# Performance work log

Hardware: AMD Instinct MI355X
Metric: run time of the kernel (lower is better)

The kernel has to match this reference:

```python
import jax, jax.numpy as jnp
import numpy as np

B, T, D = 2, 2048, 2048
H, HD, RD = 16, 192, 64
CD = HD - RD          # 128 content dims per head
QR, DL = 768, 512     # q lora rank, kv latent dim
THETA = 10000.0


def setup_inputs() -> dict:
    key = jax.random.key(0)
    ks = jax.random.split(key, 9)
    s = 0.02
    return {
        "x": jax.random.normal(ks[0], (B, T, D), jnp.float32),
        "wq_down": jax.random.normal(ks[1], (D, QR), jnp.float32) * s,
        "wq_up": jax.random.normal(ks[2], (QR, H * CD), jnp.float32) * s,
        "wq_rope": jax.random.normal(ks[3], (D, H * RD), jnp.float32) * s,
        "wkv_down": jax.random.normal(ks[4], (D, DL), jnp.float32) * s,
        "wk_up": jax.random.normal(ks[5], (DL, H * CD), jnp.float32) * s,
        "wv_up": jax.random.normal(ks[6], (DL, H * HD), jnp.float32) * s,
        "wk_rope": jax.random.normal(ks[7], (D, H * RD), jnp.float32) * s,
        "wo": jax.random.normal(ks[8], (H * HD, D), jnp.float32) * s,
    }


def _rope_tables(seq_len):
    inv = 1.0 / (THETA ** (jnp.arange(0, RD, 2, dtype=jnp.float32) / RD))  # [RD/2]
    ang = jnp.arange(seq_len, dtype=jnp.float32)[:, None] * inv[None, :]  # [T, RD/2]
    return jnp.cos(ang), jnp.sin(ang)


def _apply_rope(x, cos, sin):
    # x: [B,H,T,RD]; cos/sin: [T,RD/2] broadcast over B,H
    d = RD // 2
    x1, x2 = x[..., :d], x[..., d:]
    return jnp.concatenate([x1 * cos - x2 * sin, x1 * sin + x2 * cos], axis=-1)


def reference(x, wq_down, wq_up, wq_rope, wkv_down, wk_up, wv_up, wk_rope, wo):
    # projections
    q_c = (x @ wq_down) @ wq_up                       # [B,T,H*CD]
    q_p = x @ wq_rope                                 # [B,T,H*RD]
    latent = x @ wkv_down                             # [B,T,DL]
    k_c = latent @ wk_up                              # [B,T,H*CD]
    k_p = x @ wk_rope                                 # [B,T,H*RD]
    v = latent @ wv_up                                # [B,T,H*HD]

    def heads(t, d):
        return t.reshape(B, T, H, d).transpose(0, 2, 1, 3)  # [B,H,T,d]

    q_c, q_p = heads(q_c, CD), heads(q_p, RD)
    k_c, k_p = heads(k_c, CD), heads(k_p, RD)
    v = heads(v, HD)

    cos, sin = _rope_tables(T)
    q_p = _apply_rope(q_p, cos, sin)
    k_p = _apply_rope(k_p, cos, sin)

    q = jnp.concatenate([q_c, q_p], axis=-1)          # [B,H,T,HD]
    k = jnp.concatenate([k_c, k_p], axis=-1)          # [B,H,T,HD]

    scale = 1.0 / jnp.sqrt(jnp.asarray(HD, q.dtype))
    scores = jnp.einsum("bhqd,bhkd->bhqk", q, k) * scale
    causal = jnp.tril(jnp.ones((T, T), dtype=bool))
    scores = jnp.where(causal, scores, jnp.finfo(scores.dtype).min)
    attn = jax.nn.softmax(scores, axis=-1)
    out = jnp.einsum("bhqk,bhkd->bhqd", attn, v)      # [B,H,T,HD]
    out = out.transpose(0, 2, 1, 3).reshape(B, T, H * HD)
    return out @ wo                                   # [B,T,D]
```

## Files before the change

### kernel.cpp

```cpp
#include <hip/hip_runtime.h>
#include <hip/hip_bf16.h>
#include <cstdint>
#include <cstddef>

typedef __bf16 bf16_t;
typedef __bf16 bf16x8 __attribute__((ext_vector_type(8)));
typedef float f32x4 __attribute__((ext_vector_type(4)));

#define MFMA16(a, b, c) __builtin_amdgcn_mfma_f32_16x16x32_bf16((a), (b), (c), 0, 0, 0)

__device__ __forceinline__ void gload_lds16(const void* g, void* l) {
  __builtin_amdgcn_global_load_lds((__attribute__((address_space(1))) void*)(g),
                                   (__attribute__((address_space(3))) void*)(l),
                                   16, 0, 0);
}

__device__ __forceinline__ uint32_t pkbf(float lo, float hi) {
  union { bf16_t h[2]; uint32_t u; } u2;
  u2.h[0] = (bf16_t)lo; u2.h[1] = (bf16_t)hi;
  return u2.u;
}

__global__ __launch_bounds__(256) void cvt_f32_to_bf16(const float* __restrict__ in,
                                                       bf16_t* __restrict__ out) {
  size_t i = ((size_t)blockIdx.x * 256 + threadIdx.x) * 4;
  float4 v = *(const float4*)(in + i);
  bf16_t o[4] = {(bf16_t)v.x, (bf16_t)v.y, (bf16_t)v.z, (bf16_t)v.w};
  *(uint2*)(out + i) = *(uint2*)o;
}

__global__ __launch_bounds__(256) void transpose_all(
    const float* __restrict__ s0, const float* __restrict__ s1,
    const float* __restrict__ s2, const float* __restrict__ s3,
    const float* __restrict__ s4, const float* __restrict__ s5,
    const float* __restrict__ s6, const float* __restrict__ s7,
    bf16_t* __restrict__ t0, bf16_t* __restrict__ t1, bf16_t* __restrict__ t2,
    bf16_t* __restrict__ t3, bf16_t* __restrict__ t4, bf16_t* __restrict__ t5,
    bf16_t* __restrict__ t6, bf16_t* __restrict__ t7) {
  __shared__ bf16_t tile[32][33];
  const int lid = blockIdx.x;
  const float* src; bf16_t* dst; int R, C, bx, by;
  if (lid < 1536)       { src=s0; dst=t0; R=2048; C=768;  int lo=lid;        bx=lo%24; by=lo/24; }
  else if (lid < 2560)  { src=s1; dst=t1; R=2048; C=512;  int lo=lid-1536;   bx=lo%16; by=lo/16; }
  else if (lid < 4608)  { src=s2; dst=t2; R=2048; C=1024; int lo=lid-2560;   bx=lo%32; by=lo/32; }
  else if (lid < 6656)  { src=s3; dst=t3; R=2048; C=1024; int lo=lid-4608;   bx=lo%32; by=lo/32; }
  else if (lid < 8192)  { src=s4; dst=t4; R=768;  C=2048; int lo=lid-6656;   bx=lo%64; by=lo/64; }
  else if (lid < 9216)  { src=s5; dst=t5; R=512;  C=2048; int lo=lid-8192;   bx=lo%64; by=lo/64; }
  else if (lid < 10752) { src=s6; dst=t6; R=512;  C=3072; int lo=lid-9216;   bx=lo%96; by=lo/96; }
  else                  { src=s7; dst=t7; R=3072; C=2048; int lo=lid-10752;  bx=lo%64; by=lo/64; }
  const int c0 = bx * 32, r0 = by * 32;
  const int tx = threadIdx.x, ty = threadIdx.y;
#pragma unroll
  for (int s = 0; s < 4; s++) {
    int r = ty + s * 8;
    tile[r][tx] = (bf16_t)src[(size_t)(r0 + r) * C + c0 + tx];
  }
  __syncthreads();
#pragma unroll
  for (int s = 0; s < 4; s++) {
    int r = ty + s * 8;
    dst[(size_t)(c0 + r) * R + r0 + tx] = tile[tx][r];
  }
}

__global__ __launch_bounds__(256) void rope_both(bf16_t* __restrict__ qb,
                                                 bf16_t* __restrict__ kb) {
  const int gid = blockIdx.x;
  bf16_t* buf = (gid < 8192) ? qb : kb;
  int idx = (gid & 8191) * 256 + threadIdx.x;
  int j = idx & 31;
  int h = (idx >> 5) & 15;
  int row = idx >> 9;
  int t = row & 2047;
  size_t base = (size_t)row * 3072 + h * 192 + 128;
  float inv = expf(-(float)j * 0.28782313662425574f);
  float ang = (float)t * inv;
  float c, s;
  sincosf(ang, &s, &c);
  float x1 = (float)buf[base + j];
  float x2 = (float)buf[base + j + 32];
  buf[base + j]      = (bf16_t)(x1 * c - x2 * s);
  buf[base + j + 32] = (bf16_t)(x1 * s + x2 * c);
}

template <int MODE>
__global__ __launch_bounds__(512, 2) void gemm_bt2(const bf16_t* __restrict__ A, int lda,
                                                   const bf16_t* __restrict__ Bt,
                                                   void* __restrict__ C0, void* __restrict__ C1,
                                                   void* __restrict__ C2, int K, int ldc) {
  __shared__ __align__(16) bf16_t sA0[256 * 64];
  __shared__ __align__(16) bf16_t sB0[128 * 64];
  __shared__ __align__(16) bf16_t sA1[256 * 64];
  __shared__ __align__(16) bf16_t sB1[128 * 64];
  const int tid = threadIdx.x;
  const int l = tid & 63, w = tid >> 6;
  const int l15 = l & 15, l4 = (l >> 4) & 3;
  const int wr = w >> 1, wc = w & 1;
  const int m0 = blockIdx.y * 256, n0 = blockIdx.x * 128;
  const int nt = K >> 6;

  f32x4 acc[4][4] = {};

#define STAGEG(SA, SB, KT)                                                          \
  {                                                                                 \
    const int kts = (KT) * 64;                                                      \
    _Pragma("unroll")                                                               \
    for (int r = 0; r < 4; r++) {                                                   \
      int i = r * 512 + tid;                                                        \
      int row = i >> 3, cl = i & 7;                                                 \
      int cg = cl ^ (row & 7);                                                      \
      gload_lds16(A + (size_t)(m0 + row) * lda + kts + cg * 8,                      \
                  (char*)(SA) + (size_t)(r * 512 + w * 64) * 16);                   \
    }                                                                               \
    _Pragma("unroll")                                                               \
    for (int r = 0; r < 2; r++) {                                                   \
      int i = r * 512 + tid;                                                        \
      int row = i >> 3, cl = i & 7;                                                 \
      int cg = cl ^ (row & 7);                                                      \
      gload_lds16(Bt + (size_t)(n0 + row) * K + kts + cg * 8,                       \
                  (char*)(SB) + (size_t)(r * 512 + w * 64) * 16);                   \
    }                                                                               \
  }

#define GCOMPUTE(SA, SB)                                                            \
  {                                                                                 \
    _Pragma("unroll")                                                               \
    for (int ks = 0; ks < 2; ks++) {                                                \
      bf16x8 af[4], bfr[4];                                                         \
      _Pragma("unroll")                                                             \
      for (int mf = 0; mf < 4; mf++) {                                              \
        int row = wr * 64 + mf * 16 + l15;                                          \
        int cl = (ks * 4 + l4) ^ (row & 7);                                         \
        af[mf] = *(const bf16x8*)((SA) + row * 64 + cl * 8);                        \
      }                                                                             \
      _Pragma("unroll")                                                             \
      for (int nf = 0; nf < 4; nf++) {                                              \
        int row = wc * 64 + nf * 16 + l15;                                          \
        int cl = (ks * 4 + l4) ^ (row & 7);                                         \
        bfr[nf] = *(const bf16x8*)((SB) + row * 64 + cl * 8);                       \
      }                                                                             \
      _Pragma("unroll")                                                             \
      for (int mf = 0; mf < 4; mf++)                                                \
        _Pragma("unroll")                                                           \
        for (int nf = 0; nf < 4; nf++)                                              \
          acc[mf][nf] = MFMA16(af[mf], bfr[nf], acc[mf][nf]);                       \
    }                                                                               \
  }

  STAGEG(sA0, sB0, 0)
  for (int t = 0; t < nt; t += 2) {
    STAGEG(sA1, sB1, t + 1)
    asm volatile("s_waitcnt vmcnt(6)\n\ts_barrier" ::: "memory");
    GCOMPUTE(sA0, sB0)
    asm volatile("s_barrier" ::: "memory");
    if (t + 2 < nt) {
      STAGEG(sA0, sB0, t + 2)
      asm volatile("s_waitcnt vmcnt(6)\n\ts_barrier" ::: "memory");
    } else {
      asm volatile("s_waitcnt vmcnt(0)\n\ts_barrier" ::: "memory");
    }
    GCOMPUTE(sA1, sB1)
    asm volatile("s_barrier" ::: "memory");
  }
#undef STAGEG
#undef GCOMPUTE

#pragma unroll
  for (int mf = 0; mf < 4; mf++)
#pragma unroll
    for (int nf = 0; nf < 4; nf++) {
      const int mbase = m0 + wr * 64 + mf * 16 + l4 * 4;
      const int n = n0 + wc * 64 + nf * 16 + l15;
      if constexpr (MODE == 1) {
#pragma unroll
        for (int r = 0; r < 4; r++)
          ((float*)C0)[(size_t)(mbase + r) * ldc + n] = acc[mf][nf][r];
      } else if constexpr (MODE == 2) {
#pragma unroll
        for (int r = 0; r < 4; r++)
          ((bf16_t*)C0)[(size_t)(mbase + r) * 3072 + (n >> 7) * 192 + (n & 127)] =
              (bf16_t)acc[mf][nf][r];
      } else if constexpr (MODE == 4) {
        if (n < 1280) {
#pragma unroll
          for (int r = 0; r < 4; r++)
            ((bf16_t*)C0)[(size_t)(mbase + r) * 1280 + n] = (bf16_t)acc[mf][nf][r];
        } else if (n < 2304) {
          int nn = n - 1280;
#pragma unroll
          for (int r = 0; r < 4; r++)
            ((bf16_t*)C1)[(size_t)(mbase + r) * 3072 + (nn >> 6) * 192 + 128 + (nn & 63)] =
                (bf16_t)acc[mf][nf][r];
        } else {
          int nn = n - 2304;
#pragma unroll
          for (int r = 0; r < 4; r++)
            ((bf16_t*)C2)[(size_t)(mbase + r) * 3072 + (nn >> 6) * 192 + 128 + (nn & 63)] =
                (bf16_t)acc[mf][nf][r];
        }
      } else {
        if (n < 2048) {
#pragma unroll
          for (int r = 0; r < 4; r++)
            ((bf16_t*)C0)[(size_t)(mbase + r) * 3072 + (n >> 7) * 192 + (n & 127)] =
                (bf16_t)acc[mf][nf][r];
        } else {
          int nn = n - 2048;
          int hh = nn / 192, dd = nn - hh * 192;
          int bb = mbase >> 11, tt = mbase & 2047;
          bf16_t pk4[4] = {(bf16_t)acc[mf][nf][0], (bf16_t)acc[mf][nf][1],
                           (bf16_t)acc[mf][nf][2], (bf16_t)acc[mf][nf][3]};
          *(uint2*)((bf16_t*)C1 + ((size_t)(bb * 16 + hh) * 192 + dd) * 2048 + tt) =
              *(uint2*)pk4;
        }
      }
    }
}

__global__ __launch_bounds__(512, 2) void attn_kernel(const bf16_t* __restrict__ q,
                                                      const bf16_t* __restrict__ kbuf,
                                                      const bf16_t* __restrict__ vt,
                                                      bf16_t* __restrict__ ao) {
  __shared__ __align__(16) bf16_t sK0[64][192];
  __shared__ __align__(16) bf16_t sK1[64][192];
  __shared__ __align__(16) bf16_t sV0[192][64];
  __shared__ __align__(16) bf16_t sV1[192][64];

  const int tid = threadIdx.x, l = tid & 63, w = tid >> 6;
  const int l15 = l & 15, l4 = (l >> 4) & 3;
  const int bh = blockIdx.x & 31;
  const int c = blockIdx.x >> 5;
  const int b = bh >> 4, h = bh & 15;
  const int ca = c, cb = 15 - c;
  const int ra = ca * 128 + w * 16;
  const int rb = cb * 128 + w * 16;
  const int tga = 2 * ca + (w >> 2);
  const int tgb = 2 * cb + (w >> 2);

  const bf16_t* qp = q + (size_t)b * 2048 * 3072 + h * 192;
  const bf16_t* kp = kbuf + (size_t)b * 2048 * 3072 + h * 192;
  const bf16_t* vp = vt + (size_t)bh * 192 * 2048;

  bf16x8 qf[2][6];
#pragma unroll
  for (int kd = 0; kd < 6; kd++) {
    qf[0][kd] = *(const bf16x8*)(qp + (size_t)(ra + l15) * 3072 + kd * 32 + l4 * 8);
    qf[1][kd] = *(const bf16x8*)(qp + (size_t)(rb + l15) * 3072 + kd * 32 + l4 * 8);
  }

  f32x4 o[2][12] = {};
  float mrow[2] = {-__builtin_inff(), -__builtin_inff()};
  float lrow[2] = {0.0f, 0.0f};

  const float scale = 0.07216878364870322f;
  const float THR = 7.0f;
  const int nkt = 2 * cb + 2;
  const int src0 = l15 + ((l4 & 1) << 5);
  const int src1 = src0 + 16;
  const bool hibank = (l4 & 2) != 0;

#define STAGE(SK, SV, KT)                                                           \
  {                                                                                 \
    const int k0s = (KT) * 64;                                                      \
    _Pragma("unroll")                                                               \
    for (int r = 0; r < 3; r++) {                                                   \
      int i = r * 512 + tid;                                                        \
      int row = i / 24, cc = i % 24;                                                \
      int g = cc - (row & 7) * 3;                                                   \
      if (g < 0) g += 24;                                                           \
      gload_lds16(kp + (size_t)(k0s + row) * 3072 + g * 8,                          \
                  (char*)&SK[0][0] + (size_t)(r * 512 + w * 64) * 16);              \
    }                                                                               \
    _Pragma("unroll")                                                               \
    for (int r = 0; r < 3; r++) {                                                   \
      int i = r * 512 + tid;                                                        \
      int d = i >> 3, cc = i & 7;                                                   \
      gload_lds16(vp + (size_t)d * 2048 + k0s + (cc ^ (d & 7)) * 8,                 \
                  (char*)&SV[0][0] + (size_t)(r * 512 + w * 64) * 16);              \
    }                                                                               \
  }

#define SOFTMAX_CHUNK(c, rbase, tg)                                                    \
    {                                                                                  \
      const bool diag = (kt == (tg));                                                  \
      _Pragma("unroll")                                                                \
      for (int nf = 0; nf < 4; nf++)                                                   \
        _Pragma("unroll")                                                              \
        for (int r = 0; r < 4; r++) {                                                  \
          float sv = s[c][nf][r] * scale;                                              \
          if (diag) {                                                                  \
            int ktok = k0 + nf * 16 + l4 * 4 + r;                                      \
            if (ktok > (rbase) + l15) sv = -__builtin_inff();                          \
          }                                                                            \
          s[c][nf][r] = sv;                                                            \
        }                                                                              \
      float m_in = s[c][0][0];                                                         \
      _Pragma("unroll")                                                                \
      for (int nf = 0; nf < 4; nf++)                                                   \
        _Pragma("unroll")                                                              \
        for (int r = 0; r < 4; r++)                                                    \
          if (nf | r) m_in = fmaxf(m_in, s[c][nf][r]);                                 \
      m_in = fmaxf(m_in, __shfl_xor(m_in, 16));                                        \
      m_in = fmaxf(m_in, __shfl_xor(m_in, 32));                                        \
      if (!__all(m_in - mrow[c] <= THR)) {                                             \
        float mn = fmaxf(mrow[c], m_in);                                               \
        float alpha = __expf(mrow[c] - mn);                                            \
        mrow[c] = mn;                                                                  \
        lrow[c] *= alpha;                                                              \
        f32x4 av;                                                                      \
        _Pragma("unroll")                                                              \
        for (int r = 0; r < 4; r++) av[r] = __shfl(alpha, l4 * 4 + r);                 \
        _Pragma("unroll")                                                              \
        for (int nf2 = 0; nf2 < 12; nf2++) o[c][nf2] *= av;                            \
      }                                                                                \
      float rs = 0.0f;                                                                 \
      _Pragma("unroll")                                                                \
      for (int nf = 0; nf < 4; nf++)                                                   \
        _Pragma("unroll")                                                              \
        for (int r = 0; r < 4; r++) {                                                  \
          float pv = __expf(s[c][nf][r] - mrow[c]);                                    \
          s[c][nf][r] = pv;                                                            \
          rs += pv;                                                                    \
        }                                                                              \
      rs += __shfl_xor(rs, 16);                                                        \
      rs += __shfl_xor(rs, 32);                                                        \
      lrow[c] += rs;                                                                   \
      uint32_t wq[8];                                                                  \
      _Pragma("unroll")                                                                \
      for (int nf = 0; nf < 4; nf++) {                                                 \
        wq[nf * 2 + 0] = pkbf(s[c][nf][0], s[c][nf][1]);                               \
        wq[nf * 2 + 1] = pkbf(s[c][nf][2], s[c][nf][3]);                               \
      }                                                                                \
      _Pragma("unroll")                                                                \
      for (int ks = 0; ks < 2; ks++) {                                                 \
        uint32_t A0 = __shfl(wq[(2 * ks) * 2 + 0], src0);                              \
        uint32_t A1 = __shfl(wq[(2 * ks) * 2 + 1], src0);                              \
        uint32_t B0 = __shfl(wq[(2 * ks + 1) * 2 + 0], src0);                          \
        uint32_t B1 = __shfl(wq[(2 * ks + 1) * 2 + 1], src0);                          \
        uint32_t C0w = __shfl(wq[(2 * ks) * 2 + 0], src1);                             \
        uint32_t C1w = __shfl(wq[(2 * ks) * 2 + 1], src1);                             \
        uint32_t D0 = __shfl(wq[(2 * ks + 1) * 2 + 0], src1);                          \
        uint32_t D1 = __shfl(wq[(2 * ks + 1) * 2 + 1], src1);                          \
        union { uint32_t u[4]; bf16x8 v; } fr;                                         \
        fr.u[0] = hibank ? B0 : A0;                                                    \
        fr.u[1] = hibank ? B1 : A1;                                                    \
        fr.u[2] = hibank ? D0 : C0w;                                                   \
        fr.u[3] = hibank ? D1 : C1w;                                                   \
        pa[c][ks] = fr.v;                                                              \
      }                                                                                \
    }

#define TILE_BODY(SK, SV, KT)                                                          \
  {                                                                                    \
    const int kt = (KT);                                                               \
    const int k0 = kt * 64;                                                            \
    const bool act_a = (kt <= tga);                                                    \
    const bool act_b = (kt <= tgb);                                                    \
    f32x4 s[2][4] = {};                                                                \
    _Pragma("unroll")                                                                  \
    for (int kd = 0; kd < 6; kd++) {                                                   \
      bf16x8 bk[4];                                                                    \
      _Pragma("unroll")                                                                \
      for (int nf = 0; nf < 4; nf++) {                                                 \
        int row = nf * 16 + l15;                                                       \
        int cl = kd * 4 + l4 + (row & 7) * 3;                                          \
        if (cl >= 24) cl -= 24;                                                        \
        bk[nf] = *(const bf16x8*)(&SK[row][cl * 8]);                                   \
      }                                                                                \
      if (act_b) {                                                                     \
        _Pragma("unroll")                                                              \
        for (int nf = 0; nf < 4; nf++)                                                 \
          s[1][nf] = MFMA16(bk[nf], qf[1][kd], s[1][nf]);                              \
      }                                                                                \
      if (act_a) {                                                                     \
        _Pragma("unroll")                                                              \
        for (int nf = 0; nf < 4; nf++)                                                 \
          s[0][nf] = MFMA16(bk[nf], qf[0][kd], s[0][nf]);                              \
      }                                                                                \
    }                                                                                  \
    bf16x8 pa[2][2] = {};                                                              \
    if (act_b) SOFTMAX_CHUNK(1, rb, tgb)                                               \
    if (act_a) SOFTMAX_CHUNK(0, ra, tga)                                               \
    _Pragma("unroll")                                                                  \
    for (int ks = 0; ks < 2; ks++) {                                                   \
      _Pragma("unroll")                                                                \
      for (int nf2 = 0; nf2 < 12; nf2++) {                                             \
        int d = nf2 * 16 + l15;                                                        \
        int cl = (ks * 4 + l4) ^ (d & 7);                                              \
        bf16x8 vb = *(const bf16x8*)(&SV[d][cl * 8]);                                  \
        if (act_b) o[1][nf2] = MFMA16(pa[1][ks], vb, o[1][nf2]);                       \
        if (act_a) o[0][nf2] = MFMA16(pa[0][ks], vb, o[0][nf2]);                       \
      }                                                                                \
    }                                                                                  \
  }

  STAGE(sK0, sV0, 0)
  __syncthreads();

  for (int kt0 = 0; kt0 < nkt; kt0 += 2) {
    STAGE(sK1, sV1, kt0 + 1)
    TILE_BODY(sK0, sV0, kt0)
    __syncthreads();
    if (kt0 + 2 < nkt) STAGE(sK0, sV0, kt0 + 2)
    TILE_BODY(sK1, sV1, kt0 + 1)
    __syncthreads();
  }
#undef STAGE
#undef SOFTMAX_CHUNK
#undef TILE_BODY

#pragma unroll
  for (int mf = 0; mf < 2; mf++) {
    const int rbase = (mf == 0) ? ra : rb;
#pragma unroll
    for (int r = 0; r < 4; r++) {
      float lv = __shfl(lrow[mf], l4 * 4 + r);
      float inv = 1.0f / lv;
      int qrow = rbase + l4 * 4 + r;
#pragma unroll
      for (int nf2 = 0; nf2 < 12; nf2++) {
        int d = nf2 * 16 + l15;
        ao[(size_t)(b * 2048 + qrow) * 3072 + h * 192 + d] = (bf16_t)(o[mf][nf2][r] * inv);
      }
    }
  }
}

extern "C" void kernel_launch(void* const* d_in, const int* in_sizes, int n_in,
                              void* d_out, int out_size, void* d_ws, size_t ws_size,
                              hipStream_t stream) {
  const float* x       = (const float*)d_in[0];
  const float* wq_down = (const float*)d_in[1];
  const float* wq_up   = (const float*)d_in[2];
  const float* wq_rope = (const float*)d_in[3];
  const float* wkv_down= (const float*)d_in[4];
  const float* wk_up   = (const float*)d_in[5];
  const float* wv_up   = (const float*)d_in[6];
  const float* wk_rope = (const float*)d_in[7];
  const float* wo      = (const float*)d_in[8];
  float* out = (float*)d_out;

  char* p = (char*)d_ws;
  auto take = [&](size_t elems) { bf16_t* r = (bf16_t*)p; p += elems * 2; return r; };
  bf16_t* xb    = take(4096ull * 2048);
  bf16_t* fw1   = take(3328ull * 2048);
  bf16_t* wqu_t = take(2048ull * 768);
  bf16_t* fw2   = take(5120ull * 512);
  bf16_t* wo_t  = take(2048ull * 3072);
  bf16_t* qkvd  = take(4096ull * 1280);
  bf16_t* qbuf  = take(4096ull * 3072);
  bf16_t* kbuf  = take(4096ull * 3072);
  bf16_t* ao    = take(4096ull * 3072);
  bf16_t* vt    = take(4096ull * 3072);

  dim3 tb(32, 8);
  cvt_f32_to_bf16<<<8192, 256, 0, stream>>>(x, xb);
  transpose_all<<<16896, tb, 0, stream>>>(
      wq_down, wkv_down, wq_rope, wk_rope, wq_up, wk_up, wv_up, wo,
      fw1, fw1 + 768ull * 2048, fw1 + 1280ull * 2048, fw1 + 2304ull * 2048,
      wqu_t, fw2, fw2 + 2048ull * 512, wo_t);

  gemm_bt2<4><<<dim3(26, 16), 512, 0, stream>>>(xb, 2048, fw1, qkvd, qbuf, kbuf, 2048, 0);
  gemm_bt2<2><<<dim3(16, 16), 512, 0, stream>>>(qkvd, 1280, wqu_t, qbuf, nullptr, nullptr, 768, 0);
  gemm_bt2<5><<<dim3(40, 16), 512, 0, stream>>>(qkvd + 768, 1280, fw2, kbuf, vt, nullptr, 512, 0);

  rope_both<<<16384, 256, 0, stream>>>(qbuf, kbuf);

  attn_kernel<<<256, 512, 0, stream>>>(qbuf, kbuf, vt, ao);

  gemm_bt2<1><<<dim3(16, 16), 512, 0, stream>>>(ao, 3072, wo_t, out, nullptr, nullptr, 3072, 2048);
}
```

Measured before the change: 347.1 us.

## Triple-buffer GEMM LDS with interleaved loads and MFMA priority boosting

The GEMM main loop moves from a double-buffered scheme to a three-stage LDS ring. Each k-tile is split into four sub-phases, and the prefetch of tile t+2 is spread across those phases between barriers. s_setprio raises wave priority around the MFMA bursts in both the GEMM and the attention kernel, to encourage compute/memory overlap across waves. LDS use grows to 144 KB per block, so the launch bound of two blocks per CU may no longer hold, and the extra barriers add synchronization cost.

```diff
diff --git a/kernel.cpp b/kernel.cpp
--- a/kernel.cpp
+++ b/kernel.cpp
@@ -89,9 +89,11 @@
                                                    void* __restrict__ C0, void* __restrict__ C1,
                                                    void* __restrict__ C2, int K, int ldc) {
   __shared__ __align__(16) bf16_t sA0[256 * 64];
+  __shared__ __align__(16) bf16_t sA1[256 * 64];
+  __shared__ __align__(16) bf16_t sA2[256 * 64];
   __shared__ __align__(16) bf16_t sB0[128 * 64];
-  __shared__ __align__(16) bf16_t sA1[256 * 64];
   __shared__ __align__(16) bf16_t sB1[128 * 64];
+  __shared__ __align__(16) bf16_t sB2[128 * 64];
   const int tid = threadIdx.x;
   const int l = tid & 63, w = tid >> 6;
   const int l15 = l & 15, l4 = (l >> 4) & 3;
@@ -101,69 +103,115 @@
 
   f32x4 acc[4][4] = {};
 
-#define STAGEG(SA, SB, KT)                                                          \
-  {                                                                                 \
-    const int kts = (KT) * 64;                                                      \
-    _Pragma("unroll")                                                               \
-    for (int r = 0; r < 4; r++) {                                                   \
-      int i = r * 512 + tid;                                                        \
-      int row = i >> 3, cl = i & 7;                                                 \
-      int cg = cl ^ (row & 7);                                                      \
-      gload_lds16(A + (size_t)(m0 + row) * lda + kts + cg * 8,                      \
-                  (char*)(SA) + (size_t)(r * 512 + w * 64) * 16);                   \
-    }                                                                               \
-    _Pragma("unroll")                                                               \
-    for (int r = 0; r < 2; r++) {                                                   \
-      int i = r * 512 + tid;                                                        \
-      int row = i >> 3, cl = i & 7;                                                 \
-      int cg = cl ^ (row & 7);                                                      \
-      gload_lds16(Bt + (size_t)(n0 + row) * K + kts + cg * 8,                       \
-                  (char*)(SB) + (size_t)(r * 512 + w * 64) * 16);                   \
-    }                                                                               \
-  }
-
-#define GCOMPUTE(SA, SB)                                                            \
-  {                                                                                 \
-    _Pragma("unroll")                                                               \
-    for (int ks = 0; ks < 2; ks++) {                                                \
-      bf16x8 af[4], bfr[4];                                                         \
-      _Pragma("unroll")                                                             \
-      for (int mf = 0; mf < 4; mf++) {                                              \
-        int row = wr * 64 + mf * 16 + l15;                                          \
-        int cl = (ks * 4 + l4) ^ (row & 7);                                         \
-        af[mf] = *(const bf16x8*)((SA) + row * 64 + cl * 8);                        \
-      }                                                                             \
-      _Pragma("unroll")                                                             \
-      for (int nf = 0; nf < 4; nf++) {                                              \
-        int row = wc * 64 + nf * 16 + l15;                                          \
-        int cl = (ks * 4 + l4) ^ (row & 7);                                         \
-        bfr[nf] = *(const bf16x8*)((SB) + row * 64 + cl * 8);                       \
-      }                                                                             \
-      _Pragma("unroll")                                                             \
-      for (int mf = 0; mf < 4; mf++)                                                \
-        _Pragma("unroll")                                                           \
-        for (int nf = 0; nf < 4; nf++)                                              \
-          acc[mf][nf] = MFMA16(af[mf], bfr[nf], acc[mf][nf]);                       \
-    }                                                                               \
-  }
-
-  STAGEG(sA0, sB0, 0)
-  for (int t = 0; t < nt; t += 2) {
-    STAGEG(sA1, sB1, t + 1)
-    asm volatile("s_waitcnt vmcnt(6)\n\ts_barrier" ::: "memory");
-    GCOMPUTE(sA0, sB0)
-    asm volatile("s_barrier" ::: "memory");
-    if (t + 2 < nt) {
-      STAGEG(sA0, sB0, t + 2)
-      asm volatile("s_waitcnt vmcnt(6)\n\ts_barrier" ::: "memory");
-    } else {
-      asm volatile("s_waitcnt vmcnt(0)\n\ts_barrier" ::: "memory");
-    }
-    GCOMPUTE(sA1, sB1)
-    asm volatile("s_barrier" ::: "memory");
-  }
-#undef STAGEG
-#undef GCOMPUTE
+#define SG_A(SA, KT, R)                                                             \
+  { int i = (R) * 512 + tid; int row = i >> 3, cl = i & 7; int cg = cl ^ (row & 7); \
+    gload_lds16(A + (size_t)(m0 + row) * lda + (KT) * 64 + cg * 8,                  \
+                (char*)(SA) + (size_t)((R) * 512 + w * 64) * 16); }
+#define SG_B(SB, KT, R)                                                             \
+  { int i = (R) * 512 + tid; int row = i >> 3, cl = i & 7; int cg = cl ^ (row & 7); \
+    gload_lds16(Bt + (size_t)(n0 + row) * K + (KT) * 64 + cg * 8,                   \
+                (char*)(SB) + (size_t)((R) * 512 + w * 64) * 16); }
+#define SG_ALL(SA, SB, KT) { SG_A(SA, KT, 0) SG_A(SA, KT, 1) SG_A(SA, KT, 2) \
+                             SG_A(SA, KT, 3) SG_B(SB, KT, 0) SG_B(SB, KT, 1) }
+
+  bf16_t *a0 = sA0, *a1 = sA1, *a2 = sA2;
+  bf16_t *b0 = sB0, *b1 = sB1, *b2 = sB2;
+
+  SG_ALL(a0, b0, 0)
+  if (nt > 1) SG_ALL(a1, b1, 1)
+  asm volatile("s_waitcnt vmcnt(6)\n\ts_barrier" ::: "memory");
+
+  for (int t = 0; t < nt; ++t) {
+    const bool st = (t + 2 < nt);
+    bf16x8 af[4], bfr[4];
+
+#pragma unroll
+    for (int mf = 0; mf < 4; mf++) {
+      int row = wr * 64 + mf * 16 + l15;
+      int cl = l4 ^ (row & 7);
+      af[mf] = *(const bf16x8*)(a0 + row * 64 + cl * 8);
+    }
+#pragma unroll
+    for (int nf = 0; nf < 2; nf++) {
+      int row = wc * 64 + nf * 16 + l15;
+      int cl = l4 ^ (row & 7);
+      bfr[nf] = *(const bf16x8*)(b0 + row * 64 + cl * 8);
+    }
+    if (st) { SG_A(a2, t + 2, 0) SG_A(a2, t + 2, 1) }
+    asm volatile("s_barrier" ::: "memory");
+    __builtin_amdgcn_s_setprio(1);
+#pragma unroll
+    for (int mf = 0; mf < 4; mf++)
+#pragma unroll
+      for (int nf = 0; nf < 2; nf++)
+        acc[mf][nf] = MFMA16(af[mf], bfr[nf], acc[mf][nf]);
+    __builtin_amdgcn_s_setprio(0);
+    asm volatile("s_barrier" ::: "memory");
+
+#pragma unroll
+    for (int nf = 2; nf < 4; nf++) {
+      int row = wc * 64 + nf * 16 + l15;
+      int cl = l4 ^ (row & 7);
+      bfr[nf] = *(const bf16x8*)(b0 + row * 64 + cl * 8);
+    }
+    if (st) { SG_A(a2, t + 2, 2) SG_A(a2, t + 2, 3) }
+    asm volatile("s_barrier" ::: "memory");
+    __builtin_amdgcn_s_setprio(1);
+#pragma unroll
+    for (int mf = 0; mf < 4; mf++)
+#pragma unroll
+      for (int nf = 2; nf < 4; nf++)
+        acc[mf][nf] = MFMA16(af[mf], bfr[nf], acc[mf][nf]);
+    __builtin_amdgcn_s_setprio(0);
+    asm volatile("s_barrier" ::: "memory");
+
+#pragma unroll
+    for (int mf = 0; mf < 4; mf++) {
+      int row = wr * 64 + mf * 16 + l15;
+      int cl = (4 + l4) ^ (row & 7);
+      af[mf] = *(const bf16x8*)(a0 + row * 64 + cl * 8);
+    }
+#pragma unroll
+    for (int nf = 0; nf < 2; nf++) {
+      int row = wc * 64 + nf * 16 + l15;
+      int cl = (4 + l4) ^ (row & 7);
+      bfr[nf] = *(const bf16x8*)(b0 + row * 64 + cl * 8);
+    }
+    if (st) { SG_B(b2, t + 2, 0) SG_B(b2, t + 2, 1) }
+    asm volatile("s_barrier" ::: "memory");
+    __builtin_amdgcn_s_setprio(1);
+#pragma unroll
+    for (int mf = 0; mf < 4; mf++)
+#pragma unroll
+      for (int nf = 0; nf < 2; nf++)
+        acc[mf][nf] = MFMA16(af[mf], bfr[nf], acc[mf][nf]);
+    __builtin_amdgcn_s_setprio(0);
+    asm volatile("s_barrier" ::: "memory");
+
+#pragma unroll
+    for (int nf = 2; nf < 4; nf++) {
+      int row = wc * 64 + nf * 16 + l15;
+      int cl = (4 + l4) ^ (row & 7);
+      bfr[nf] = *(const bf16x8*)(b0 + row * 64 + cl * 8);
+    }
+    asm volatile("s_barrier" ::: "memory");
+    __builtin_amdgcn_s_setprio(1);
+#pragma unroll
+    for (int mf = 0; mf < 4; mf++)
+#pragma unroll
+      for (int nf = 2; nf < 4; nf++)
+        acc[mf][nf] = MFMA16(af[mf], bfr[nf], acc[mf][nf]);
+    __builtin_amdgcn_s_setprio(0);
+    if (st) asm volatile("s_waitcnt vmcnt(6)" ::: "memory");
+    else    asm volatile("s_waitcnt vmcnt(0)" ::: "memory");
+    asm volatile("s_barrier" ::: "memory");
+
+    bf16_t* ta = a0; a0 = a1; a1 = a2; a2 = ta;
+    bf16_t* tb = b0; b0 = b1; b1 = b2; b2 = tb;
+  }
+#undef SG_A
+#undef SG_B
+#undef SG_ALL
 
 #pragma unroll
   for (int mf = 0; mf < 4; mf++)
@@ -357,6 +405,7 @@
     const bool act_a = (kt <= tga);                                                    \
     const bool act_b = (kt <= tgb);                                                    \
     f32x4 s[2][4] = {};                                                                \
+    __builtin_amdgcn_s_setprio(1);                                                     \
     _Pragma("unroll")                                                                  \
     for (int kd = 0; kd < 6; kd++) {                                                   \
       bf16x8 bk[4];                                                                    \
@@ -378,9 +427,11 @@
           s[0][nf] = MFMA16(bk[nf], qf[0][kd], s[0][nf]);                              \
       }                                                                                \
     }                                                                                  \
+    __builtin_amdgcn_s_setprio(0);                                                     \
     bf16x8 pa[2][2] = {};                                                              \
     if (act_b) SOFTMAX_CHUNK(1, rb, tgb)                                               \
     if (act_a) SOFTMAX_CHUNK(0, ra, tga)                                               \
+    __builtin_amdgcn_s_setprio(1);                                                     \
     _Pragma("unroll")                                                                  \
     for (int ks = 0; ks < 2; ks++) {                                                   \
       _Pragma("unroll")                                                                \
@@ -392,6 +443,7 @@
         if (act_a) o[0][nf2] = MFMA16(pa[0][ks], vb, o[0][nf2]);                       \
       }                                                                                \
     }                                                                                  \
+    __builtin_amdgcn_s_setprio(0);                                                     \
   }
 
   STAGE(sK0, sV0, 0)
```

Result: no change. 341.3 us (-1.7%).
